# Optimization experiments

Measured on AMD Instinct MI355X. Metric: run time of the kernel, lower is better.

The kernel has to match this reference:

```python
import jax, jax.numpy as jnp
import numpy as np

PATCH = 7          # patch_size (stride fixed to 1, loop=False)
ALPHA = 0.01       # coherent_alpha


def extract_patches(x, p):
    # x: [1, C, T] -> [n, C*p], n = T - p + 1  (unfold over time, stride 1)
    b, c, t = x.shape
    n = t - p + 1
    idx = jnp.arange(n)[:, None] + jnp.arange(p)[None, :]   # [n, p]
    patches = x[0][:, idx]                                   # [C, n, p]
    return patches.transpose(1, 0, 2).reshape(n, c * p)      # [n, C*p]


def setup_inputs() -> dict:
    key = jax.random.key(0)
    kx, ky = jax.random.split(key)
    X = jax.random.normal(kx, (1, 72, 8192), dtype=jnp.float32)
    Y = jax.random.normal(ky, (1, 72, 8192), dtype=jnp.float32)
    return {"X": X, "Y": Y}


def reference(X, Y):
    p = PATCH
    b, c, t = X.shape
    d = c * p
    xp = extract_patches(X, p)                               # [n1, d]
    yp = extract_patches(Y, p)                               # [n2, d]
    # efficient_cdist: squared L2 distances, normalized by patch dim d
    dist = ((xp * xp).sum(1)[:, None] + (yp * yp).sum(1)[None, :]
            - 2.0 * (xp @ yp.T)) / d                         # [n1, n2]
    # coherent_alpha: bidirectional-similarity normalization by per-y-patch min
    norm_dist = dist / (ALPHA + dist.min(axis=0, keepdims=True))
    nnf = jnp.argmin(norm_dist, axis=1)                      # [n1] int
    dists = jnp.take_along_axis(dist, nnf[:, None], axis=1)[:, 0]
    # combine_patches: gather matched y patches, overlap-add (fold), normalize by counts
    matched = yp[nnf].reshape(-1, c, p)                      # [n1, C, p]
    n1 = matched.shape[0]
    idx = jnp.arange(n1)[:, None] + jnp.arange(p)[None, :]   # [n1, p] -> time index
    acc = jnp.zeros((c, t), X.dtype).at[:, idx].add(matched.transpose(1, 0, 2))
    cnt = jnp.zeros((t,), X.dtype).at[idx].add(jnp.ones((n1, p), X.dtype))
    blended = (acc / cnt)[None]                              # [1, C, T]
    return blended, dists.mean()
```

## Files before the change

kernel.cpp:

```cpp
#include <hip/hip_runtime.h>
#include <stdint.h>

#define TT 8192
#define CC 72
#define PP 7
#define NN (TT - PP + 1)
#define DD (CC * PP)

#define TI 122
#define SG 128
#define SPAD 132
#define NTILE ((NN + TI - 1) / TI)

#define STAGE_BYTES (CC * SG * 4)
#define SMEM_UNION  (2 * STAGE_BYTES)

#define TAIL_BYTES 196608

#define SROWS 4

constexpr float INV_D = 1.0f / (float)DD;
constexpr float ALPHA_C = 0.01f;
constexpr float QSCALE = 67108864.0f;

__global__ void prep_kernel(const float* __restrict__ X, const float* __restrict__ Y,
                            float* __restrict__ sx, float* __restrict__ sy,
                            unsigned* __restrict__ colmin,
                            unsigned long long* __restrict__ packed,
                            unsigned long long* __restrict__ qsum) {
    int i = blockIdx.x * 256 + threadIdx.x;
    if (blockIdx.y == 0) {
        if (i == 0) *qsum = 0ULL;
        if (i < TT) { colmin[i] = 0x7f800000u; packed[i] = ~0ULL; }
        if (i < NN) {
            float ax = 0.0f;
            for (int c = 0; c < CC; ++c) {
                const float* xr = X + c * TT + i;
#pragma unroll
                for (int k = 0; k < PP; ++k) { float v = xr[k]; ax += v * v; }
            }
            sx[i] = ax;
        }
    } else {
        if (i < NN) {
            float ay = 0.0f;
            for (int c = 0; c < CC; ++c) {
                const float* yr = Y + c * TT + i;
#pragma unroll
                for (int k = 0; k < PP; ++k) { float w = yr[k]; ay += w * w; }
            }
            sy[i] = ay;
        }
    }
}

__device__ __forceinline__ void tile_dots256(const float* __restrict__ X,
                                             const float* __restrict__ Y,
                                             int i0, int j0, char* smem,
                                             float dot[8][8]) {
    float (*Xs)[SG]   = (float (*)[SG])smem;
    float (*Ys)[SG]   = (float (*)[SG])(smem + STAGE_BYTES);
    float (*Sl)[SPAD] = (float (*)[SPAD])smem;
    const int tid = threadIdx.x;

    for (int idx = tid; idx < CC * SG / 2; idx += 256) {
        int c  = idx >> 6;
        int t2 = (idx & 63) * 2;
        int gx = i0 + t2, gy = j0 + t2;
        float2 xv, yv;
        if (gx + 1 < TT) xv = *(const float2*)(X + c * TT + gx);
        else { xv.x = X[c * TT + min(gx, TT - 1)]; xv.y = X[c * TT + min(gx + 1, TT - 1)]; }
        if (gy + 1 < TT) yv = *(const float2*)(Y + c * TT + gy);
        else { yv.x = Y[c * TT + min(gy, TT - 1)]; yv.y = Y[c * TT + min(gy + 1, TT - 1)]; }
        *(float2*)&Xs[c][t2] = xv;
        *(float2*)&Ys[c][t2] = yv;
    }
    __syncthreads();

    const int su = tid >> 4, sv = tid & 15;
    float s[8][8];
#pragma unroll
    for (int a = 0; a < 8; ++a)
#pragma unroll
        for (int b = 0; b < 8; ++b) s[a][b] = 0.0f;

#pragma unroll 4
    for (int c = 0; c < CC; ++c) {
        float xv[8], yv[8];
        *(float4*)&xv[0] = *(const float4*)&Xs[c][su * 8];
        *(float4*)&xv[4] = *(const float4*)&Xs[c][su * 8 + 4];
        *(float4*)&yv[0] = *(const float4*)&Ys[c][sv * 4];
        *(float4*)&yv[4] = *(const float4*)&Ys[c][64 + sv * 4];
#pragma unroll
        for (int a = 0; a < 8; ++a)
#pragma unroll
            for (int b = 0; b < 8; ++b)
                s[a][b] += xv[a] * yv[b];
    }
    __syncthreads();

#pragma unroll
    for (int a = 0; a < 8; ++a) {
        int row = su * 8 + a;
        int swz = ((row >> 3) & 3) << 2;
        *(float4*)&Sl[row][(sv * 4) ^ swz]      = make_float4(s[a][0], s[a][1], s[a][2], s[a][3]);
        *(float4*)&Sl[row][(64 + sv * 4) ^ swz] = make_float4(s[a][4], s[a][5], s[a][6], s[a][7]);
    }
    __syncthreads();

    const int ri = (tid >> 4) * 8, rj = (tid & 15) * 8;
#pragma unroll
    for (int a = 0; a < 8; ++a)
#pragma unroll
        for (int b = 0; b < 8; ++b) dot[a][b] = 0.0f;

#pragma unroll
    for (int r = 0; r < 14; ++r) {
        int row = ri + r;
        int swz = ((row >> 3) & 3) << 2;
        float f[14];
        *(float4*)&f[0]  = *(const float4*)&Sl[row][(rj)      ^ swz];
        *(float4*)&f[4]  = *(const float4*)&Sl[row][(rj + 4)  ^ swz];
        *(float4*)&f[8]  = *(const float4*)&Sl[row][(rj + 8)  ^ swz];
        *(float2*)&f[12] = *(const float2*)&Sl[row][(rj + 12) ^ swz];
#pragma unroll
        for (int a = 0; a < 8; ++a) {
            const int k = r - a;
            if (k >= 0 && k < PP) {
#pragma unroll
                for (int b = 0; b < 8; ++b)
                    dot[a][b] += f[b + k];
            }
        }
    }
}

__global__ __launch_bounds__(256) void pass1_k(
        const float* __restrict__ X, const float* __restrict__ Y,
        const float* __restrict__ sx, const float* __restrict__ sy,
        unsigned* __restrict__ colmin,
        float* __restrict__ distbuf, int storeTiles) {
    __shared__ __align__(16) char smem[SMEM_UNION + 1024];
    unsigned* cmin_s = (unsigned*)(smem + SMEM_UNION);

    const int i0 = blockIdx.y * TI;
    const int j0 = blockIdx.x * TI;
    const int tid = threadIdx.x;
    const bool store = ((int)blockIdx.y < storeTiles);
    if (tid < 128) cmin_s[tid] = 0x7f800000u;

    float dot[8][8];
    tile_dots256(X, Y, i0, j0, smem, dot);

    const int ri = (tid >> 4) * 8, rj = (tid & 15) * 8;
    const int gj0 = j0 + rj;

    bool bv[8]; float syv[8];
#pragma unroll
    for (int b = 0; b < 8; ++b) {
        int lj = rj + b, gj = gj0 + b;
        bv[b] = (lj < TI && gj < NN);
        syv[b] = bv[b] ? sy[gj] : 0.0f;
    }
    const bool fullCols = (rj + 7 < TI) && (gj0 + 7 < NN);
    const bool al16 = ((gj0 & 3) == 0);

    float cm[8];
#pragma unroll
    for (int b = 0; b < 8; ++b) cm[b] = __uint_as_float(0x7f800000u);

#pragma unroll
    for (int a = 0; a < 8; ++a) {
        int li = ri + a, gi = i0 + li;
        if (li >= TI || gi >= NN) continue;
        float sxi = sx[gi];
        float d8[8];
#pragma unroll
        for (int b = 0; b < 8; ++b) {
            d8[b] = (sxi + syv[b] - 2.0f * dot[a][b]) * INV_D;
            if (bv[b]) cm[b] = fminf(cm[b], d8[b]);
        }
        if (store) {
            float* drow = distbuf + (size_t)gi * TT + gj0;
            if (fullCols) {
                if (al16) {
                    *(float4*)&drow[0] = make_float4(d8[0], d8[1], d8[2], d8[3]);
                    *(float4*)&drow[4] = make_float4(d8[4], d8[5], d8[6], d8[7]);
                } else {
                    *(float2*)&drow[0] = make_float2(d8[0], d8[1]);
                    *(float4*)&drow[2] = make_float4(d8[2], d8[3], d8[4], d8[5]);
                    *(float2*)&drow[6] = make_float2(d8[6], d8[7]);
                }
            } else {
#pragma unroll
                for (int b = 0; b < 8; ++b)
                    if (bv[b]) drow[b] = d8[b];
            }
        }
    }
#pragma unroll
    for (int b = 0; b < 8; ++b)
        if (bv[b]) atomicMin(&cmin_s[rj + b], __float_as_uint(cm[b]));
    __syncthreads();
    if (tid < TI) {
        int gj = j0 + tid;
        if (gj < NN) atomicMin(&colmin[gj], cmin_s[tid]);
    }
}

template<bool FULL>
__global__ __launch_bounds__(256) void pass2_stream_k(
        const float* __restrict__ distbuf, const unsigned* __restrict__ colmin,
        unsigned long long* __restrict__ packed,
        int* __restrict__ nnf, unsigned long long* __restrict__ qsum, int nrows) {
    const int i0 = blockIdx.x * SROWS;
    const float* row0 = distbuf + (size_t)i0 * TT;
    const float* cmf = (const float*)colmin;

    unsigned long long best[SROWS];
#pragma unroll
    for (int r = 0; r < SROWS; ++r) best[r] = ~0ULL;

    for (int jb = threadIdx.x * 8; jb < NN; jb += 2048) {
        float4 c4a = *(const float4*)(cmf + jb);
        float4 c4b = *(const float4*)(cmf + jb + 4);
        float acm[8];
#pragma unroll
        for (int e = 0; e < 8; ++e)
            acm[e] = ALPHA_C + ((e < 4) ? (&c4a.x)[e] : (&c4b.x)[e - 4]);
#pragma unroll
        for (int r = 0; r < SROWS; ++r) {
            const float* row = row0 + (size_t)r * TT;
            float4 d4a = *(const float4*)(row + jb);
            float4 d4b = *(const float4*)(row + jb + 4);
#pragma unroll
            for (int e = 0; e < 8; ++e) {
                int j = jb + e;
                if (j < NN) {
                    float d  = (e < 4) ? (&d4a.x)[e] : (&d4b.x)[e - 4];
                    float nd = d / acm[e];
                    unsigned long long pk =
                        ((unsigned long long)__float_as_uint(nd) << 32) | (unsigned)j;
                    best[r] = (pk < best[r]) ? pk : best[r];
                }
            }
        }
    }
#pragma unroll
    for (int r = 0; r < SROWS; ++r)
#pragma unroll
        for (int off = 32; off > 0; off >>= 1) {
            unsigned long long o = __shfl_down(best[r], off, 64);
            best[r] = (o < best[r]) ? o : best[r];
        }
    __shared__ unsigned long long wb[4][SROWS];
    int lane = threadIdx.x & 63, wid = threadIdx.x >> 6;
    if (lane == 0) {
#pragma unroll
        for (int r = 0; r < SROWS; ++r) wb[wid][r] = best[r];
    }
    __syncthreads();
    if (threadIdx.x < SROWS) {
        int r = threadIdx.x;
        int i = i0 + r;
        if (i < nrows) {
            unsigned long long b0 = wb[0][r];
            b0 = (wb[1][r] < b0) ? wb[1][r] : b0;
            b0 = (wb[2][r] < b0) ? wb[2][r] : b0;
            b0 = (wb[3][r] < b0) ? wb[3][r] : b0;
            if (FULL) {
                int j = (int)(b0 & 0xffffffffu);
                nnf[i] = j;
                float dval = distbuf[(size_t)i * TT + j];
                atomicAdd(qsum, (unsigned long long)(long long)(dval * QSCALE));
            } else {
                packed[i] = b0;
            }
        }
    }
}

__global__ __launch_bounds__(256) void pass2_k(
        const float* __restrict__ X, const float* __restrict__ Y,
        const float* __restrict__ sx, const float* __restrict__ sy,
        const unsigned* __restrict__ colmin,
        unsigned long long* __restrict__ packed, int itile_ofs) {
    __shared__ __align__(16) char smem[SMEM_UNION + 1024];
    unsigned long long* pmin_s = (unsigned long long*)(smem + SMEM_UNION);

    const int i0 = (itile_ofs + blockIdx.y) * TI;
    const int j0 = blockIdx.x * TI;
    const int tid = threadIdx.x;
    if (tid < TI) pmin_s[tid] = ~0ULL;

    float dot[8][8];
    tile_dots256(X, Y, i0, j0, smem, dot);

    const int ri = (tid >> 4) * 8, rj = (tid & 15) * 8;
    const int gj0 = j0 + rj;

    bool bv[8]; float syv[8], acm[8];
#pragma unroll
    for (int b = 0; b < 8; ++b) {
        int lj = rj + b, gj = gj0 + b;
        bv[b] = (lj < TI && gj < NN);
        syv[b] = bv[b] ? sy[gj] : 0.0f;
        acm[b] = bv[b] ? (ALPHA_C + __uint_as_float(colmin[gj])) : 1.0f;
    }

#pragma unroll
    for (int a = 0; a < 8; ++a) {
        int li = ri + a, gi = i0 + li;
        if (li >= TI || gi >= NN) continue;
        float sxi = sx[gi];
        unsigned long long best = ~0ULL;
#pragma unroll
        for (int b = 0; b < 8; ++b) {
            if (bv[b]) {
                float d  = (sxi + syv[b] - 2.0f * dot[a][b]) * INV_D;
                float nd = d / acm[b];
                unsigned long long pk =
                    ((unsigned long long)__float_as_uint(nd) << 32) | (unsigned)(gj0 + b);
                best = (pk < best) ? pk : best;
            }
        }
        atomicMin(&pmin_s[li], best);
    }
    __syncthreads();
    if (tid < TI) {
        int gi = i0 + tid;
        if (gi < NN) atomicMin(&packed[gi], pmin_s[tid]);
    }
}

__global__ void finalize_kernel(const float* __restrict__ X, const float* __restrict__ Y,
                                const float* __restrict__ sx, const float* __restrict__ sy,
                                const unsigned long long* __restrict__ packed,
                                int* __restrict__ nnf, unsigned long long* __restrict__ qsum) {
    int i = blockIdx.x * 256 + threadIdx.x;
    long long q = 0;
    if (i < NN) {
        int j = (int)(packed[i] & 0xffffffffu);
        nnf[i] = j;
        float dot = 0.0f;
        for (int c = 0; c < CC; ++c) {
            const float* xr = X + c * TT + i;
            const float* yr = Y + c * TT + j;
#pragma unroll
            for (int k = 0; k < PP; ++k) dot += xr[k] * yr[k];
        }
        float dval = (sx[i] + sy[j] - 2.0f * dot) * INV_D;
        q = (long long)(dval * QSCALE);
    }
    __shared__ long long red[256];
    red[threadIdx.x] = q;
    __syncthreads();
    for (int s = 128; s > 0; s >>= 1) {
        if (threadIdx.x < s) red[threadIdx.x] += red[threadIdx.x + s];
        __syncthreads();
    }
    if (threadIdx.x == 0) atomicAdd(qsum, (unsigned long long)red[0]);
}

__global__ void fold_kernel(const float* __restrict__ Y, const int* __restrict__ nnf,
                            const unsigned long long* __restrict__ qsum,
                            float* __restrict__ out) {
    int idx = blockIdx.x * 256 + threadIdx.x;
    if (idx < CC * TT) {
        int c = idx >> 13;
        int t = idx & (TT - 1);
        float acc = 0.0f;
        int cnt = 0;
#pragma unroll
        for (int k = 0; k < PP; ++k) {
            int i = t - k;
            if (i >= 0 && i < NN) {
                acc += Y[c * TT + nnf[i] + k];
                cnt++;
            }
        }
        out[idx] = acc / (float)cnt;
    }
    if (idx == 0) {
        double m = (double)*qsum * (1.0 / (double)QSCALE) / (double)NN;
        out[CC * TT] = (float)m;
    }
}

extern "C" void kernel_launch(void* const* d_in, const int* in_sizes, int n_in,
                              void* d_out, int out_size, void* d_ws, size_t ws_size,
                              hipStream_t stream) {
    const float* X = (const float*)d_in[0];
    const float* Y = (const float*)d_in[1];
    float* out = (float*)d_out;

    char* w = (char*)d_ws;
    size_t base = 0;
    if (ws_size > TAIL_BYTES) base = ((ws_size - TAIL_BYTES) / 32768) * 32768;
    unsigned long long* packed = (unsigned long long*)(w + base);
    unsigned*           colmin = (unsigned*)(w + base + 65536);
    float*              sx     = (float*)(w + base + 98304);
    float*              sy     = (float*)(w + base + 131072);
    int*                nnf    = (int*)(w + base + 163840);
    unsigned long long* qsum   = (unsigned long long*)(w + base + 196600);
    float*              distbuf = (float*)w;

    const long storeRows = (long)(base / ((size_t)TT * 4));
    int storeTiles = 0;
    for (int nT = 1; nT <= NTILE; ++nT) {
        long need = (long)nT * TI; if (need > NN) need = NN;
        if (need <= storeRows) storeTiles = nT; else break;
    }
    const int SR = (storeTiles * TI < NN) ? storeTiles * TI : NN;
    const bool full = (storeTiles >= NTILE);

    prep_kernel<<<dim3((TT + 255) / 256, 2), 256, 0, stream>>>(X, Y, sx, sy, colmin, packed, qsum);

    dim3 grid(NTILE, NTILE);
    pass1_k<<<grid, 256, 0, stream>>>(X, Y, sx, sy, colmin, distbuf, storeTiles);

    if (full) {
        pass2_stream_k<true><<<(NN + SROWS - 1) / SROWS, 256, 0, stream>>>(
            distbuf, colmin, packed, nnf, qsum, NN);
    } else {
        if (SR > 0)
            pass2_stream_k<false><<<(SR + SROWS - 1) / SROWS, 256, 0, stream>>>(
                distbuf, colmin, packed, nnf, qsum, SR);
        if (storeTiles < NTILE) {
            dim3 grid2(NTILE, NTILE - storeTiles);
            pass2_k<<<grid2, 256, 0, stream>>>(X, Y, sx, sy, colmin, packed, storeTiles);
        }
        finalize_kernel<<<(NN + 255) / 256, 256, 0, stream>>>(X, Y, sx, sy, packed, nnf, qsum);
    }
    fold_kernel<<<(CC * TT + 255) / 256, 256, 0, stream>>>(Y, nnf, qsum, out);
}
```

Measured before the change: 296.9 us.

## Make pass1 persistent with atomic tile ticket and register prefetch of next tile

Pass1 becomes a persistent kernel with 512 blocks that pull tiles from an atomic ticket counter. While a block runs the shift-add epilogue for the current tile, it prefetches the next tile's X and Y slices into registers (18 float2 pairs per thread), hiding global load latency. This costs extra registers (72 more VGPRs), which may lower occupancy, and adds a serialising atomic per tile.

After: 388.4 us. +30.8%, slower.

```diff
diff --git a/kernel.cpp b/kernel.cpp
--- a/kernel.cpp
+++ b/kernel.cpp
@@ -11,6 +11,7 @@
 #define SG 128
 #define SPAD 132
 #define NTILE ((NN + TI - 1) / TI)
+#define NT2   (NTILE * NTILE)
 
 #define STAGE_BYTES (CC * SG * 4)
 #define SMEM_UNION  (2 * STAGE_BYTES)
@@ -18,6 +19,7 @@
 #define TAIL_BYTES 196608
 
 #define SROWS 4
+#define NPF 18
 
 constexpr float INV_D = 1.0f / (float)DD;
 constexpr float ALPHA_C = 0.01f;
@@ -27,10 +29,11 @@
                             float* __restrict__ sx, float* __restrict__ sy,
                             unsigned* __restrict__ colmin,
                             unsigned long long* __restrict__ packed,
-                            unsigned long long* __restrict__ qsum) {
+                            unsigned long long* __restrict__ qsum,
+                            unsigned* __restrict__ ticket) {
     int i = blockIdx.x * 256 + threadIdx.x;
     if (blockIdx.y == 0) {
-        if (i == 0) *qsum = 0ULL;
+        if (i == 0) { *qsum = 0ULL; *ticket = 0u; }
         if (i < TT) { colmin[i] = 0x7f800000u; packed[i] = ~0ULL; }
         if (i < NN) {
             float ax = 0.0f;
@@ -54,16 +57,13 @@
     }
 }
 
-__device__ __forceinline__ void tile_dots256(const float* __restrict__ X,
-                                             const float* __restrict__ Y,
-                                             int i0, int j0, char* smem,
-                                             float dot[8][8]) {
-    float (*Xs)[SG]   = (float (*)[SG])smem;
-    float (*Ys)[SG]   = (float (*)[SG])(smem + STAGE_BYTES);
-    float (*Sl)[SPAD] = (float (*)[SPAD])smem;
-    const int tid = threadIdx.x;
-
-    for (int idx = tid; idx < CC * SG / 2; idx += 256) {
+__device__ __forceinline__ void stage_prefetch(const float* __restrict__ X,
+                                               const float* __restrict__ Y,
+                                               int i0, int j0, int tid,
+                                               float2 px[NPF], float2 py[NPF]) {
+#pragma unroll
+    for (int k = 0; k < NPF; ++k) {
+        int idx = tid + k * 256;
         int c  = idx >> 6;
         int t2 = (idx & 63) * 2;
         int gx = i0 + t2, gy = j0 + t2;
@@ -72,66 +72,7 @@
         else { xv.x = X[c * TT + min(gx, TT - 1)]; xv.y = X[c * TT + min(gx + 1, TT - 1)]; }
         if (gy + 1 < TT) yv = *(const float2*)(Y + c * TT + gy);
         else { yv.x = Y[c * TT + min(gy, TT - 1)]; yv.y = Y[c * TT + min(gy + 1, TT - 1)]; }
-        *(float2*)&Xs[c][t2] = xv;
-        *(float2*)&Ys[c][t2] = yv;
-    }
-    __syncthreads();
-
-    const int su = tid >> 4, sv = tid & 15;
-    float s[8][8];
-#pragma unroll
-    for (int a = 0; a < 8; ++a)
-#pragma unroll
-        for (int b = 0; b < 8; ++b) s[a][b] = 0.0f;
-
-#pragma unroll 4
-    for (int c = 0; c < CC; ++c) {
-        float xv[8], yv[8];
-        *(float4*)&xv[0] = *(const float4*)&Xs[c][su * 8];
-        *(float4*)&xv[4] = *(const float4*)&Xs[c][su * 8 + 4];
-        *(float4*)&yv[0] = *(const float4*)&Ys[c][sv * 4];
-        *(float4*)&yv[4] = *(const float4*)&Ys[c][64 + sv * 4];
-#pragma unroll
-        for (int a = 0; a < 8; ++a)
-#pragma unroll
-            for (int b = 0; b < 8; ++b)
-                s[a][b] += xv[a] * yv[b];
-    }
-    __syncthreads();
-
-#pragma unroll
-    for (int a = 0; a < 8; ++a) {
-        int row = su * 8 + a;
-        int swz = ((row >> 3) & 3) << 2;
-        *(float4*)&Sl[row][(sv * 4) ^ swz]      = make_float4(s[a][0], s[a][1], s[a][2], s[a][3]);
-        *(float4*)&Sl[row][(64 + sv * 4) ^ swz] = make_float4(s[a][4], s[a][5], s[a][6], s[a][7]);
-    }
-    __syncthreads();
-
-    const int ri = (tid >> 4) * 8, rj = (tid & 15) * 8;
-#pragma unroll
-    for (int a = 0; a < 8; ++a)
-#pragma unroll
-        for (int b = 0; b < 8; ++b) dot[a][b] = 0.0f;
-
-#pragma unroll
-    for (int r = 0; r < 14; ++r) {
-        int row = ri + r;
-        int swz = ((row >> 3) & 3) << 2;
-        float f[14];
-        *(float4*)&f[0]  = *(const float4*)&Sl[row][(rj)      ^ swz];
-        *(float4*)&f[4]  = *(const float4*)&Sl[row][(rj + 4)  ^ swz];
-        *(float4*)&f[8]  = *(const float4*)&Sl[row][(rj + 8)  ^ swz];
-        *(float2*)&f[12] = *(const float2*)&Sl[row][(rj + 12) ^ swz];
-#pragma unroll
-        for (int a = 0; a < 8; ++a) {
-            const int k = r - a;
-            if (k >= 0 && k < PP) {
-#pragma unroll
-                for (int b = 0; b < 8; ++b)
-                    dot[a][b] += f[b + k];
-            }
-        }
+        px[k] = xv; py[k] = yv;
     }
 }
 
@@ -139,72 +80,168 @@
         const float* __restrict__ X, const float* __restrict__ Y,
         const float* __restrict__ sx, const float* __restrict__ sy,
         unsigned* __restrict__ colmin,
-        float* __restrict__ distbuf, int storeTiles) {
+        float* __restrict__ distbuf, int storeTiles,
+        unsigned* __restrict__ ticket) {
     __shared__ __align__(16) char smem[SMEM_UNION + 1024];
+    __shared__ int tile_s;
     unsigned* cmin_s = (unsigned*)(smem + SMEM_UNION);
 
-    const int i0 = blockIdx.y * TI;
-    const int j0 = blockIdx.x * TI;
+    float (*Xs)[SG]   = (float (*)[SG])smem;
+    float (*Ys)[SG]   = (float (*)[SG])(smem + STAGE_BYTES);
+    float (*Sl)[SPAD] = (float (*)[SPAD])smem;
+
     const int tid = threadIdx.x;
-    const bool store = ((int)blockIdx.y < storeTiles);
-    if (tid < 128) cmin_s[tid] = 0x7f800000u;
-
-    float dot[8][8];
-    tile_dots256(X, Y, i0, j0, smem, dot);
-
-    const int ri = (tid >> 4) * 8, rj = (tid & 15) * 8;
-    const int gj0 = j0 + rj;
-
-    bool bv[8]; float syv[8];
-#pragma unroll
-    for (int b = 0; b < 8; ++b) {
-        int lj = rj + b, gj = gj0 + b;
-        bv[b] = (lj < TI && gj < NN);
-        syv[b] = bv[b] ? sy[gj] : 0.0f;
-    }
-    const bool fullCols = (rj + 7 < TI) && (gj0 + 7 < NN);
-    const bool al16 = ((gj0 & 3) == 0);
-
-    float cm[8];
-#pragma unroll
-    for (int b = 0; b < 8; ++b) cm[b] = __uint_as_float(0x7f800000u);
-
-#pragma unroll
-    for (int a = 0; a < 8; ++a) {
-        int li = ri + a, gi = i0 + li;
-        if (li >= TI || gi >= NN) continue;
-        float sxi = sx[gi];
-        float d8[8];
+    const int su = tid >> 4, sv = tid & 15;
+    const int ri = su * 8, rj = sv * 8;
+
+    if (tid == 0) tile_s = (int)atomicAdd(ticket, 1u);
+    __syncthreads();
+    int tile = tile_s;
+    bool valid = (tile < NT2);
+
+    float2 px[NPF], py[NPF];
+    if (valid) {
+        int by = tile / NTILE, bx = tile - by * NTILE;
+        stage_prefetch(X, Y, by * TI, bx * TI, tid, px, py);
+    }
+
+    while (valid) {
+        const int by = tile / NTILE, bx = tile - by * NTILE;
+        const int i0 = by * TI, j0 = bx * TI;
+        const bool store = (by < storeTiles);
+
+        __syncthreads();
+        if (tid < 128) cmin_s[tid] = 0x7f800000u;
+
+#pragma unroll
+        for (int k = 0; k < NPF; ++k) {
+            int idx = tid + k * 256;
+            int c  = idx >> 6;
+            int t2 = (idx & 63) * 2;
+            *(float2*)&Xs[c][t2] = px[k];
+            *(float2*)&Ys[c][t2] = py[k];
+        }
+        __syncthreads();
+
+        float s[8][8];
+#pragma unroll
+        for (int a = 0; a < 8; ++a)
+#pragma unroll
+            for (int b = 0; b < 8; ++b) s[a][b] = 0.0f;
+
+#pragma unroll 4
+        for (int c = 0; c < CC; ++c) {
+            float xv[8], yv[8];
+            *(float4*)&xv[0] = *(const float4*)&Xs[c][su * 8];
+            *(float4*)&xv[4] = *(const float4*)&Xs[c][su * 8 + 4];
+            *(float4*)&yv[0] = *(const float4*)&Ys[c][sv * 4];
+            *(float4*)&yv[4] = *(const float4*)&Ys[c][64 + sv * 4];
+#pragma unroll
+            for (int a = 0; a < 8; ++a)
+#pragma unroll
+                for (int b = 0; b < 8; ++b)
+                    s[a][b] += xv[a] * yv[b];
+        }
+        __syncthreads();
+
+        if (tid == 0) tile_s = (int)atomicAdd(ticket, 1u);
+
+#pragma unroll
+        for (int a = 0; a < 8; ++a) {
+            int row = su * 8 + a;
+            int swz = ((row >> 3) & 3) << 2;
+            *(float4*)&Sl[row][(sv * 4) ^ swz]      = make_float4(s[a][0], s[a][1], s[a][2], s[a][3]);
+            *(float4*)&Sl[row][(64 + sv * 4) ^ swz] = make_float4(s[a][4], s[a][5], s[a][6], s[a][7]);
+        }
+        __syncthreads();
+
+        const int ntile = tile_s;
+        const bool nvalid = (ntile < NT2);
+        if (nvalid) {
+            int nby = ntile / NTILE, nbx = ntile - nby * NTILE;
+            stage_prefetch(X, Y, nby * TI, nbx * TI, tid, px, py);
+        }
+
+        float dot[8][8];
+#pragma unroll
+        for (int a = 0; a < 8; ++a)
+#pragma unroll
+            for (int b = 0; b < 8; ++b) dot[a][b] = 0.0f;
+
+#pragma unroll
+        for (int r = 0; r < 14; ++r) {
+            int row = ri + r;
+            int swz = ((row >> 3) & 3) << 2;
+            float f[14];
+            *(float4*)&f[0]  = *(const float4*)&Sl[row][(rj)      ^ swz];
+            *(float4*)&f[4]  = *(const float4*)&Sl[row][(rj + 4)  ^ swz];
+            *(float4*)&f[8]  = *(const float4*)&Sl[row][(rj + 8)  ^ swz];
+            *(float2*)&f[12] = *(const float2*)&Sl[row][(rj + 12) ^ swz];
+#pragma unroll
+            for (int a = 0; a < 8; ++a) {
+                const int k = r - a;
+                if (k >= 0 && k < PP) {
+#pragma unroll
+                    for (int b = 0; b < 8; ++b)
+                        dot[a][b] += f[b + k];
+                }
+            }
+        }
+
+        const int gj0 = j0 + rj;
+        bool bv[8]; float syv[8];
 #pragma unroll
         for (int b = 0; b < 8; ++b) {
-            d8[b] = (sxi + syv[b] - 2.0f * dot[a][b]) * INV_D;
-            if (bv[b]) cm[b] = fminf(cm[b], d8[b]);
-        }
-        if (store) {
-            float* drow = distbuf + (size_t)gi * TT + gj0;
-            if (fullCols) {
-                if (al16) {
-                    *(float4*)&drow[0] = make_float4(d8[0], d8[1], d8[2], d8[3]);
-                    *(float4*)&drow[4] = make_float4(d8[4], d8[5], d8[6], d8[7]);
+            int lj = rj + b, gj = gj0 + b;
+            bv[b] = (lj < TI && gj < NN);
+            syv[b] = bv[b] ? sy[gj] : 0.0f;
+        }
+        const bool fullCols = (rj + 7 < TI) && (gj0 + 7 < NN);
+        const bool al16 = ((gj0 & 3) == 0);
+
+        float cm[8];
+#pragma unroll
+        for (int b = 0; b < 8; ++b) cm[b] = __uint_as_float(0x7f800000u);
+
+#pragma unroll
+        for (int a = 0; a < 8; ++a) {
+            int li = ri + a, gi = i0 + li;
+            if (li >= TI || gi >= NN) continue;
+            float sxi = sx[gi];
+            float d8[8];
+#pragma unroll
+            for (int b = 0; b < 8; ++b) {
+                d8[b] = (sxi + syv[b] - 2.0f * dot[a][b]) * INV_D;
+                if (bv[b]) cm[b] = fminf(cm[b], d8[b]);
+            }
+            if (store) {
+                float* drow = distbuf + (size_t)gi * TT + gj0;
+                if (fullCols) {
+                    if (al16) {
+                        *(float4*)&drow[0] = make_float4(d8[0], d8[1], d8[2], d8[3]);
+                        *(float4*)&drow[4] = make_float4(d8[4], d8[5], d8[6], d8[7]);
+                    } else {
+                        *(float2*)&drow[0] = make_float2(d8[0], d8[1]);
+                        *(float4*)&drow[2] = make_float4(d8[2], d8[3], d8[4], d8[5]);
+                        *(float2*)&drow[6] = make_float2(d8[6], d8[7]);
+                    }
                 } else {
-                    *(float2*)&drow[0] = make_float2(d8[0], d8[1]);
-                    *(float4*)&drow[2] = make_float4(d8[2], d8[3], d8[4], d8[5]);
-                    *(float2*)&drow[6] = make_float2(d8[6], d8[7]);
+#pragma unroll
+                    for (int b = 0; b < 8; ++b)
+                        if (bv[b]) drow[b] = d8[b];
                 }
-            } else {
-#pragma unroll
-                for (int b = 0; b < 8; ++b)
-                    if (bv[b]) drow[b] = d8[b];
-            }
-        }
-    }
-#pragma unroll
-    for (int b = 0; b < 8; ++b)
-        if (bv[b]) atomicMin(&cmin_s[rj + b], __float_as_uint(cm[b]));
-    __syncthreads();
-    if (tid < TI) {
-        int gj = j0 + tid;
-        if (gj < NN) atomicMin(&colmin[gj], cmin_s[tid]);
+            }
+        }
+#pragma unroll
+        for (int b = 0; b < 8; ++b)
+            if (bv[b]) atomicMin(&cmin_s[rj + b], __float_as_uint(cm[b]));
+        __syncthreads();
+        if (tid < TI) {
+            int gj = j0 + tid;
+            if (gj < NN) atomicMin(&colmin[gj], cmin_s[tid]);
+        }
+
+        tile = ntile; valid = nvalid;
     }
 }
 
@@ -280,6 +317,87 @@
     }
 }
 
+__device__ __forceinline__ void tile_dots256(const float* __restrict__ X,
+                                             const float* __restrict__ Y,
+                                             int i0, int j0, char* smem,
+                                             float dot[8][8]) {
+    float (*Xs)[SG]   = (float (*)[SG])smem;
+    float (*Ys)[SG]   = (float (*)[SG])(smem + STAGE_BYTES);
+    float (*Sl)[SPAD] = (float (*)[SPAD])smem;
+    const int tid = threadIdx.x;
+
+    for (int idx = tid; idx < CC * SG / 2; idx += 256) {
+        int c  = idx >> 6;
+        int t2 = (idx & 63) * 2;
+        int gx = i0 + t2, gy = j0 + t2;
+        float2 xv, yv;
+        if (gx + 1 < TT) xv = *(const float2*)(X + c * TT + gx);
+        else { xv.x = X[c * TT + min(gx, TT - 1)]; xv.y = X[c * TT + min(gx + 1, TT - 1)]; }
+        if (gy + 1 < TT) yv = *(const float2*)(Y + c * TT + gy);
+        else { yv.x = Y[c * TT + min(gy, TT - 1)]; yv.y = Y[c * TT + min(gy + 1, TT - 1)]; }
+        *(float2*)&Xs[c][t2] = xv;
+        *(float2*)&Ys[c][t2] = yv;
+    }
+    __syncthreads();
+
+    const int su = tid >> 4, sv = tid & 15;
+    float s[8][8];
+#pragma unroll
+    for (int a = 0; a < 8; ++a)
+#pragma unroll
+        for (int b = 0; b < 8; ++b) s[a][b] = 0.0f;
+
+#pragma unroll 4
+    for (int c = 0; c < CC; ++c) {
+        float xv[8], yv[8];
+        *(float4*)&xv[0] = *(const float4*)&Xs[c][su * 8];
+        *(float4*)&xv[4] = *(const float4*)&Xs[c][su * 8 + 4];
+        *(float4*)&yv[0] = *(const float4*)&Ys[c][sv * 4];
+        *(float4*)&yv[4] = *(const float4*)&Ys[c][64 + sv * 4];
+#pragma unroll
+        for (int a = 0; a < 8; ++a)
+#pragma unroll
+            for (int b = 0; b < 8; ++b)
+                s[a][b] += xv[a] * yv[b];
+    }
+    __syncthreads();
+
+#pragma unroll
+    for (int a = 0; a < 8; ++a) {
+        int row = su * 8 + a;
+        int swz = ((row >> 3) & 3) << 2;
+        *(float4*)&Sl[row][(sv * 4) ^ swz]      = make_float4(s[a][0], s[a][1], s[a][2], s[a][3]);
+        *(float4*)&Sl[row][(64 + sv * 4) ^ swz] = make_float4(s[a][4], s[a][5], s[a][6], s[a][7]);
+    }
+    __syncthreads();
+
+    const int ri = (tid >> 4) * 8, rj = (tid & 15) * 8;
+#pragma unroll
+    for (int a = 0; a < 8; ++a)
+#pragma unroll
+        for (int b = 0; b < 8; ++b) dot[a][b] = 0.0f;
+
+#pragma unroll
+    for (int r = 0; r < 14; ++r) {
+        int row = ri + r;
+        int swz = ((row >> 3) & 3) << 2;
+        float f[14];
+        *(float4*)&f[0]  = *(const float4*)&Sl[row][(rj)      ^ swz];
+        *(float4*)&f[4]  = *(const float4*)&Sl[row][(rj + 4)  ^ swz];
+        *(float4*)&f[8]  = *(const float4*)&Sl[row][(rj + 8)  ^ swz];
+        *(float2*)&f[12] = *(const float2*)&Sl[row][(rj + 12) ^ swz];
+#pragma unroll
+        for (int a = 0; a < 8; ++a) {
+            const int k = r - a;
+            if (k >= 0 && k < PP) {
+#pragma unroll
+                for (int b = 0; b < 8; ++b)
+                    dot[a][b] += f[b + k];
+            }
+        }
+    }
+}
+
 __global__ __launch_bounds__(256) void pass2_k(
         const float* __restrict__ X, const float* __restrict__ Y,
         const float* __restrict__ sx, const float* __restrict__ sy,
@@ -402,6 +520,7 @@
     float*              sx     = (float*)(w + base + 98304);
     float*              sy     = (float*)(w + base + 131072);
     int*                nnf    = (int*)(w + base + 163840);
+    unsigned*           ticket = (unsigned*)(w + base + 196592);
     unsigned long long* qsum   = (unsigned long long*)(w + base + 196600);
     float*              distbuf = (float*)w;
 
@@ -414,10 +533,10 @@
     const int SR = (storeTiles * TI < NN) ? storeTiles * TI : NN;
     const bool full = (storeTiles >= NTILE);
 
-    prep_kernel<<<dim3((TT + 255) / 256, 2), 256, 0, stream>>>(X, Y, sx, sy, colmin, packed, qsum);
-
-    dim3 grid(NTILE, NTILE);
-    pass1_k<<<grid, 256, 0, stream>>>(X, Y, sx, sy, colmin, distbuf, storeTiles);
+    prep_kernel<<<dim3((TT + 255) / 256, 2), 256, 0, stream>>>(
+        X, Y, sx, sy, colmin, packed, qsum, ticket);
+
+    pass1_k<<<512, 256, 0, stream>>>(X, Y, sx, sy, colmin, distbuf, storeTiles, ticket);
 
     if (full) {
         pass2_stream_k<true><<<(NN + SROWS - 1) / SROWS, 256, 0, stream>>>(
```
